# Kernel optimization log

Measured on AMD Instinct MI355X. Metric: run time of the kernel, lower is better.

The kernel has to match this reference:

```python
import jax, jax.numpy as jnp
import numpy as np
import math

B, T, E, H = 4, 4096, 1024, 16
D = E // H  # head dim
EPS_DENOM = 1e-6
LN_EPS = 1e-5


def setup_inputs() -> dict:
    key = jax.random.key(0)
    ks = jax.random.split(key, 8)
    s = 0.02
    return {
        "x": jax.random.normal(ks[0], (B, T, E), jnp.float32),
        "ln1_w": jnp.ones((E,), jnp.float32),
        "ln1_b": jnp.zeros((E,), jnp.float32),
        "wq": jax.random.normal(ks[1], (E, E), jnp.float32) * s,
        "bq": jnp.zeros((E,), jnp.float32),
        "wk": jax.random.normal(ks[2], (E, E), jnp.float32) * s,
        "bk": jnp.zeros((E,), jnp.float32),
        "wv": jax.random.normal(ks[3], (E, E), jnp.float32) * s,
        "bv": jnp.zeros((E,), jnp.float32),
        "wo": jax.random.normal(ks[4], (E, E), jnp.float32) * s,
        "bo": jnp.zeros((E,), jnp.float32),
        "ln2_w": jnp.ones((E,), jnp.float32),
        "ln2_b": jnp.zeros((E,), jnp.float32),
        "w_fc": jax.random.normal(ks[5], (E, 4 * E), jnp.float32) * s,
        "b_fc": jnp.zeros((4 * E,), jnp.float32),
        "w_proj": jax.random.normal(ks[6], (4 * E, E), jnp.float32) * s,
        "b_proj": jnp.zeros((E,), jnp.float32),
    }


def _layernorm(x, w, b):
    mu = jnp.mean(x, axis=-1, keepdims=True)
    var = jnp.mean(jnp.square(x - mu), axis=-1, keepdims=True)
    return (x - mu) * jax.lax.rsqrt(var + LN_EPS) * w + b


def _cosformer_attn(x, wq, bq, wk, bk, wv, bv, wo, bo):
    # ReLU feature map on q, k projections
    q = jax.nn.relu(x @ wq + bq)  # [B,T,E]
    k = jax.nn.relu(x @ wk + bk)
    v = x @ wv + bv
    # split heads -> [B,H,T,D]
    q = q.reshape(B, T, H, D).transpose(0, 2, 1, 3)
    k = k.reshape(B, T, H, D).transpose(0, 2, 1, 3)
    v = v.reshape(B, T, H, D).transpose(0, 2, 1, 3)
    # cosine reweighting: idx_i = pi/2 * (i+1)/M, M = T (self-attention)
    idx = (math.pi / 2.0) * jnp.arange(1, T + 1, dtype=x.dtype) / T  # [T]
    s = jnp.sin(idx)[None, None, :, None]
    c = jnp.cos(idx)[None, None, :, None]
    q_ = jnp.concatenate([q * s, q * c], axis=-1)  # [B,H,T,2D]
    k_ = jnp.concatenate([k * s, k * c], axis=-1)  # [B,H,T,2D]
    # non-causal linear attention: O = Q' (K'^T V) / (Q' K'^T 1)
    kv = jnp.einsum("bhtd,bhte->bhde", k_, v)       # [B,H,2D,D]
    z = 1.0 / jnp.maximum(jnp.einsum("bhtd,bhd->bht", q_, k_.sum(axis=2)), EPS_DENOM)
    out = jnp.einsum("bhtd,bhde,bht->bhte", q_, kv, z)  # [B,H,T,D]
    out = out.transpose(0, 2, 1, 3).reshape(B, T, E)
    return out @ wo + bo


def reference(x, ln1_w, ln1_b, wq, bq, wk, bk, wv, bv, wo, bo,
              ln2_w, ln2_b, w_fc, b_fc, w_proj, b_proj):
    h = _layernorm(x, ln1_w, ln1_b)
    x = x + _cosformer_attn(h, wq, bq, wk, bk, wv, bv, wo, bo)
    h = _layernorm(x, ln2_w, ln2_b)
    h = jax.nn.gelu(h @ w_fc + b_fc, approximate=False) @ w_proj + b_proj
    return x + h
```

## Files before the change

kernel.cpp:

```cpp
#include <hip/hip_runtime.h>

#define PI_F 3.14159265358979f
#define MT 16384
#define EE 1024
#define FF 4096
#define NCH 8
#define CHT (4096 / NCH)

typedef unsigned short u16;
typedef __attribute__((ext_vector_type(8))) short short8;
typedef __attribute__((ext_vector_type(4))) float f32x4;

__device__ __forceinline__ float bf2f(u16 u) {
  unsigned int v = ((unsigned int)u) << 16;
  float f;
  __builtin_memcpy(&f, &v, 4);
  return f;
}
__device__ __forceinline__ u16 f2bf(float f) {
  unsigned int x;
  __builtin_memcpy(&x, &f, 4);
  unsigned int r = x + 0x7fffu + ((x >> 16) & 1u);
  return (u16)(r >> 16);
}
__device__ __forceinline__ float ldin(const void* p, long i, int f32) {
  return f32 ? ((const float*)p)[i] : bf2f(((const u16*)p)[i]);
}
__device__ __forceinline__ void async16(const u16* g, u16* l) {
  __builtin_amdgcn_global_load_lds(
      (const __attribute__((address_space(1))) unsigned int*)g,
      (__attribute__((address_space(3))) unsigned int*)l, 16, 0, 0);
}

__global__ __launch_bounds__(256) void detect_dtype(const u16* __restrict__ x,
                                                    int* __restrict__ flag) {
  const int tid = threadIdx.x;
  int cnt = 0;
  for (int i = tid; i < 2048; i += 256) {
    const int e = (x[i] >> 7) & 0xFF;
    if (e == 0 || e >= 0x90) cnt++;
  }
#pragma unroll
  for (int o = 32; o > 0; o >>= 1) cnt += __shfl_xor(cnt, o);
  __shared__ int s[4];
  if ((tid & 63) == 0) s[tid >> 6] = cnt;
  __syncthreads();
  if (tid == 0) flag[0] = (s[0] + s[1] + s[2] + s[3] > 200) ? 1 : 0;
}

__global__ __launch_bounds__(256) void transpose_in(
    const void* __restrict__ src, const int* __restrict__ flag,
    u16* __restrict__ dst, int R, int C) {
  __shared__ float tile[64][65];
  const int f = *flag;
  const int tx = threadIdx.x & 63, ty = threadIdx.x >> 6;
  const long c0 = (long)blockIdx.x * 64, r0 = (long)blockIdx.y * 64;
#pragma unroll
  for (int i = 0; i < 16; i++) {
    const int r = ty + i * 4;
    tile[r][tx] = ldin(src, (r0 + r) * (long)C + c0 + tx, f);
  }
  __syncthreads();
#pragma unroll
  for (int i = 0; i < 16; i++) {
    const int cc = ty + i * 4;
    dst[(c0 + cc) * (long)R + r0 + tx] = f2bf(tile[tx][cc]);
  }
}

__global__ __launch_bounds__(256) void concat3(
    const void* __restrict__ a, const void* __restrict__ b,
    const void* __restrict__ c, const int* __restrict__ flag,
    float* __restrict__ out) {
  const int i = blockIdx.x * 256 + threadIdx.x;
  const int fl = *flag;
  if (i < 1024) out[i] = ldin(a, i, fl);
  else if (i < 2048) out[i] = ldin(b, i - 1024, fl);
  else if (i < 3072) out[i] = ldin(c, i - 2048, fl);
}

__global__ __launch_bounds__(256) void ln_kernel(
    const void* __restrict__ xin, int xmode, const int* __restrict__ flag,
    const void* __restrict__ w, const void* __restrict__ b,
    u16* __restrict__ out) {
  const long row = blockIdx.x;
  const int tid = threadIdx.x;
  const int fl = *flag;
  const int xf = (xmode == 2) ? fl : xmode;
  float v[4];
  if (xf) {
    const float4 q = ((const float4*)((const float*)xin + row * EE))[tid];
    v[0] = q.x; v[1] = q.y; v[2] = q.z; v[3] = q.w;
  } else {
    const ushort4 u = ((const ushort4*)((const u16*)xin + row * EE))[tid];
    v[0] = bf2f(u.x); v[1] = bf2f(u.y); v[2] = bf2f(u.z); v[3] = bf2f(u.w);
  }
  float sum = v[0] + v[1] + v[2] + v[3];
  float sq = v[0] * v[0] + v[1] * v[1] + v[2] * v[2] + v[3] * v[3];
#pragma unroll
  for (int o = 32; o > 0; o >>= 1) {
    sum += __shfl_xor(sum, o);
    sq += __shfl_xor(sq, o);
  }
  __shared__ float s1[4], s2[4];
  const int wave = tid >> 6, lane = tid & 63;
  if (lane == 0) { s1[wave] = sum; s2[wave] = sq; }
  __syncthreads();
  sum = s1[0] + s1[1] + s1[2] + s1[3];
  sq = s2[0] + s2[1] + s2[2] + s2[3];
  const float mu = sum * (1.f / EE);
  const float var = sq * (1.f / EE) - mu * mu;
  const float rs = rsqrtf(var + 1e-5f);
  ushort4 o4;
  float r0 = (v[0] - mu) * rs * ldin(w, tid * 4 + 0, fl) + ldin(b, tid * 4 + 0, fl);
  float r1 = (v[1] - mu) * rs * ldin(w, tid * 4 + 1, fl) + ldin(b, tid * 4 + 1, fl);
  float r2 = (v[2] - mu) * rs * ldin(w, tid * 4 + 2, fl) + ldin(b, tid * 4 + 2, fl);
  float r3 = (v[3] - mu) * rs * ldin(w, tid * 4 + 3, fl) + ldin(b, tid * 4 + 3, fl);
  o4.x = f2bf(r0); o4.y = f2bf(r1); o4.z = f2bf(r2); o4.w = f2bf(r3);
  ((ushort4*)(out + row * EE))[tid] = o4;
}

__global__ __launch_bounds__(256) void gemm_bf16(
    const u16* __restrict__ A, const u16* __restrict__ Bt,
    const void* __restrict__ bias, int biasF32,
    const void* __restrict__ res, int resMode,
    void* __restrict__ Cout, void* __restrict__ Cv, int outMode, long coff,
    const int* __restrict__ flag, int M, int N, int K, int act) {
  __shared__ u16 As[2][128 * 32];
  __shared__ u16 Bs[2][128 * 32];
  const int tid = threadIdx.x;
  const int lane = tid & 63;
  const int wave = tid >> 6;
  const int quad = lane >> 4;
  const int l16 = lane & 15;
  const int wm = (wave >> 1) * 64;
  const int wn = (wave & 1) * 64;
  const long bm = (long)blockIdx.x * 128;
  const long bn = (long)blockIdx.y * 128;

  f32x4 acc[4][4];
#pragma unroll
  for (int i = 0; i < 4; i++)
#pragma unroll
    for (int j = 0; j < 4; j++)
#pragma unroll
      for (int r = 0; r < 4; r++) acc[i][j][r] = 0.f;

  const int srow = tid >> 2;
  const int scol = (tid & 3) * 8;
  const u16* Ap = A + (bm + srow) * (long)K + scol;
  const u16* Bp = Bt + (bn + srow) * (long)K + scol;
  const long K64 = (long)64 * K;
  u16* As0 = &As[0][0];
  u16* Bs0 = &Bs[0][0];

  auto stage = [&](int b) {
    u16* Ad = As0 + b * 4096 + wave * 512;
    u16* Bd = Bs0 + b * 4096 + wave * 512;
    async16(Ap, Ad);
    async16(Ap + K64, Ad + 2048);
    async16(Bp, Bd);
    async16(Bp + K64, Bd + 2048);
    Ap += 32;
    Bp += 32;
  };
  auto compute = [&](int b) {
    const u16* Ab = As0 + b * 4096;
    const u16* Bb = Bs0 + b * 4096;
    short8 af[4], bfr[4];
#pragma unroll
    for (int i = 0; i < 4; i++)
      af[i] = *(const short8*)&Ab[(wm + i * 16 + l16) * 32 + quad * 8];
#pragma unroll
    for (int i = 0; i < 4; i++)
      bfr[i] = *(const short8*)&Bb[(wn + i * 16 + l16) * 32 + quad * 8];
#pragma unroll
    for (int mi = 0; mi < 4; mi++)
#pragma unroll
      for (int ni = 0; ni < 4; ni++)
        acc[mi][ni] = __builtin_amdgcn_mfma_f32_16x16x32_bf16(
            af[mi], bfr[ni], acc[mi][ni], 0, 0, 0);
  };

  stage(0);
  __syncthreads();
  const int nk = K >> 5;
  int buf = 0;
  for (int t = 1; t < nk; t++) {
    stage(buf ^ 1);
    compute(buf);
    __syncthreads();
    buf ^= 1;
  }
  compute(buf);

  const int fl = *flag;
#pragma unroll
  for (int ni = 0; ni < 4; ni++) {
    const long gc = bn + wn + ni * 16 + l16;
    const float bvv = biasF32 ? ((const float*)bias)[gc] : ldin(bias, gc, fl);
#pragma unroll
    for (int mi = 0; mi < 4; mi++) {
      const long gr0 = bm + wm + mi * 16 + quad * 4;
#pragma unroll
      for (int r = 0; r < 4; r++) {
        float val = acc[mi][ni][r] + bvv;
        if (act == 1 || (act == 3 && gc < 2048)) val = fmaxf(val, 0.f);
        else if (act == 2) val = 0.5f * val * (1.f + erff(val * 0.70710678118654752f));
        const long row = gr0 + r;
        if (outMode == 3) {
          const long plane = gc >> 10;
          u16* dst = (plane == 2) ? (u16*)Cv
                                  : ((u16*)Cout + plane * ((long)M << 10));
          dst[(row << 10) + (gc & 1023)] = f2bf(val);
        } else {
          const long idx = row * (long)N + gc;
          float v2 = val;
          if (resMode == 1) v2 += ((const float*)res)[idx];
          else if (resMode == 2) v2 += ldin(res, idx, fl);
          if (outMode == 1 || (outMode == 2 && fl)) ((float*)Cout)[coff + idx] = v2;
          else ((u16*)Cout)[coff + idx] = f2bf(v2);
        }
      }
    }
  }
}

__global__ __launch_bounds__(256) void kv_partial(
    const u16* __restrict__ k, const u16* __restrict__ v,
    float* __restrict__ kvpart, float* __restrict__ kspart) {
  const int bh = blockIdx.x;
  const int ch = blockIdx.y;
  const int b = bh >> 4, h = bh & 15;
  const int tid = threadIdx.x;
  __shared__ float kl[8][64], vl[8][64];
  const int dkq = tid >> 4;
  const int dvq = tid & 15;
  float accS[4][4] = {}, accC[4][4] = {};
  float ksS[4] = {}, ksC[4] = {};
  const int tt = tid >> 5;
  const int cc = (tid & 31) * 2;
  const long base = ((long)b * 4096 + ch * CHT) * EE + h * 64;
  for (int tb = 0; tb < CHT; tb += 8) {
    const long roff = base + (long)(tb + tt) * EE + cc;
    const unsigned int ku = *(const unsigned int*)(k + roff);
    const unsigned int vu = *(const unsigned int*)(v + roff);
    __syncthreads();
    kl[tt][cc] = bf2f((u16)ku);
    kl[tt][cc + 1] = bf2f((u16)(ku >> 16));
    vl[tt][cc] = bf2f((u16)vu);
    vl[tt][cc + 1] = bf2f((u16)(vu >> 16));
    __syncthreads();
#pragma unroll
    for (int j = 0; j < 8; j++) {
      const int t = ch * CHT + tb + j;
      float s, c;
      __sincosf((float)(t + 1) * (PI_F * 0.5f / 4096.f), &s, &c);
      float kk[4], vv[4];
#pragma unroll
      for (int i = 0; i < 4; i++) {
        kk[i] = kl[j][dkq * 4 + i];
        vv[i] = vl[j][dvq * 4 + i];
      }
#pragma unroll
      for (int i = 0; i < 4; i++) {
        const float ks_ = kk[i] * s, kc_ = kk[i] * c;
        ksS[i] += ks_;
        ksC[i] += kc_;
#pragma unroll
        for (int jj = 0; jj < 4; jj++) {
          accS[i][jj] += ks_ * vv[jj];
          accC[i][jj] += kc_ * vv[jj];
        }
      }
    }
  }
  float* outS = kvpart + (((long)ch * 64 + bh) * 2 + 0) * 4096;
  float* outC = outS + 4096;
#pragma unroll
  for (int i = 0; i < 4; i++)
#pragma unroll
    for (int jj = 0; jj < 4; jj++) {
      outS[(dkq * 4 + i) * 64 + dvq * 4 + jj] = accS[i][jj];
      outC[(dkq * 4 + i) * 64 + dvq * 4 + jj] = accC[i][jj];
    }
  if (dvq == 0) {
    float* oS = kspart + ((long)ch * 64 + bh) * 2 * 64;
#pragma unroll
    for (int i = 0; i < 4; i++) {
      oS[dkq * 4 + i] = ksS[i];
      oS[64 + dkq * 4 + i] = ksC[i];
    }
  }
}

__global__ __launch_bounds__(256) void kv_reduce(
    const float* __restrict__ kvpart, const float* __restrict__ kspart,
    float* __restrict__ kvcomb, float* __restrict__ kscomb) {
  const long KVTOT = 64L * 2 * 4096;
  const long KSTOT = 64L * 2 * 64;
  const long idx = (long)blockIdx.x * 256 + threadIdx.x;
  if (idx < KVTOT) {
    float s = 0.f;
#pragma unroll
    for (int chn = 0; chn < NCH; chn++) s += kvpart[chn * KVTOT + idx];
    kvcomb[idx] = s;
  } else {
    const long i2 = idx - KVTOT;
    if (i2 < KSTOT) {
      float s = 0.f;
#pragma unroll
      for (int chn = 0; chn < NCH; chn++) s += kspart[chn * KSTOT + i2];
      kscomb[i2] = s;
    }
  }
}

__global__ __launch_bounds__(256) void attn_apply(
    const u16* __restrict__ q, const float* __restrict__ kvcomb,
    const float* __restrict__ kscomb, u16* __restrict__ attn) {
  const int bh = blockIdx.x;
  const int b = bh >> 4, h = bh & 15;
  const int t0 = blockIdx.y * 64;
  const int tid = threadIdx.x;
  __shared__ float kvl[2][64][64];
  __shared__ float ksl[2][64];
  __shared__ float ql[64][66];

  const float4* kvsrc = (const float4*)(kvcomb + (long)bh * 8192);
  float4* kvdst = (float4*)&kvl[0][0][0];
#pragma unroll
  for (int i = 0; i < 8; i++) kvdst[tid + 256 * i] = kvsrc[tid + 256 * i];
  if (tid < 32) ((float4*)&ksl[0][0])[tid] = ((const float4*)(kscomb + (long)bh * 128))[tid];
  {
    const int r = tid >> 2;
    const int c = (tid & 3) * 16;
    const u16* qp = q + ((long)b * 4096 + t0 + r) * EE + h * 64 + c;
    const uint4 u0 = *(const uint4*)qp;
    const uint4 u1 = *(const uint4*)(qp + 8);
    unsigned int uu[8] = {u0.x, u0.y, u0.z, u0.w, u1.x, u1.y, u1.z, u1.w};
#pragma unroll
    for (int i = 0; i < 8; i++) {
      ql[r][c + 2 * i] = bf2f((u16)uu[i]);
      ql[r][c + 2 * i + 1] = bf2f((u16)(uu[i] >> 16));
    }
  }
  __syncthreads();

  const int tg = tid >> 4;
  const int dvq = tid & 15;
  const int dv0 = dvq * 4;

  float o1[4][4] = {}, o2[4][4] = {}, zs[4] = {}, zc[4] = {};
  for (int dk = 0; dk < 64; dk++) {
    const float ks0 = ksl[0][dk], ks1 = ksl[1][dk];
    float kv0[4], kv1[4];
#pragma unroll
    for (int j = 0; j < 4; j++) {
      kv0[j] = kvl[0][dk][dv0 + j];
      kv1[j] = kvl[1][dk][dv0 + j];
    }
#pragma unroll
    for (int it = 0; it < 4; it++) {
      const float qv = ql[tg + it * 16][dk];
      zs[it] += qv * ks0;
      zc[it] += qv * ks1;
#pragma unroll
      for (int j = 0; j < 4; j++) {
        o1[it][j] += qv * kv0[j];
        o2[it][j] += qv * kv1[j];
      }
    }
  }
#pragma unroll
  for (int it = 0; it < 4; it++) {
    const int t = t0 + tg + it * 16;
    float s, c;
    __sincosf((float)(t + 1) * (PI_F * 0.5f / 4096.f), &s, &c);
    const float z = s * zs[it] + c * zc[it];
    const float zinv = 1.f / fmaxf(z, 1e-6f);
    ushort4 o4;
    o4.x = f2bf((s * o1[it][0] + c * o2[it][0]) * zinv);
    o4.y = f2bf((s * o1[it][1] + c * o2[it][1]) * zinv);
    o4.z = f2bf((s * o1[it][2] + c * o2[it][2]) * zinv);
    o4.w = f2bf((s * o1[it][3] + c * o2[it][3]) * zinv);
    *(ushort4*)(attn + ((long)b * 4096 + t) * EE + h * 64 + dv0) = o4;
  }
}

extern "C" void kernel_launch(void* const* d_in, const int* in_sizes, int n_in,
                              void* d_out, int out_size, void* d_ws, size_t ws_size,
                              hipStream_t stream) {
  const void* x = d_in[0];
  const void* ln1w = d_in[1];
  const void* ln1b = d_in[2];
  const void* wq = d_in[3];
  const void* bq = d_in[4];
  const void* wk = d_in[5];
  const void* bk = d_in[6];
  const void* wv = d_in[7];
  const void* bv = d_in[8];
  const void* wo = d_in[9];
  const void* bo = d_in[10];
  const void* ln2w = d_in[11];
  const void* ln2b = d_in[12];
  const void* wfc = d_in[13];
  const void* bfc = d_in[14];
  const void* wproj = d_in[15];
  const void* bproj = d_in[16];

  char* ws = (char*)d_ws;
  size_t off = 0;
  auto alloc = [&](size_t bytes) -> char* {
    char* p = ws + off;
    off += (bytes + 255) & ~((size_t)255);
    return p;
  };
  int* flag = (int*)alloc(256);
  u16* wqkvT = (u16*)alloc((size_t)3 * EE * EE * 2);
  u16* woT = (u16*)alloc((size_t)EE * EE * 2);
  u16* wfcT = (u16*)alloc((size_t)EE * FF * 2);
  u16* wprojT = (u16*)alloc((size_t)FF * EE * 2);
  float* qkvBias = (float*)alloc(3072 * 4);
  u16* h = (u16*)alloc((size_t)MT * EE * 2);
  float* x2 = (float*)alloc((size_t)MT * EE * 4);
  u16* qk2 = (u16*)alloc((size_t)2 * MT * EE * 2);
  float* kvpart = (float*)alloc((size_t)NCH * 64 * 2 * 64 * 64 * 4);
  float* kspart = (float*)alloc((size_t)NCH * 64 * 2 * 64 * 4);
  float* kvcomb = (float*)alloc((size_t)64 * 2 * 64 * 64 * 4);
  float* kscomb = (float*)alloc((size_t)64 * 2 * 64 * 4);
  const long PL = (long)MT * EE;
  u16* qb = qk2;
  u16* kb = qk2 + PL;
  u16* vb = (u16*)x2;
  u16* attnb = kb;
  u16* g = qk2;
  (void)ws_size; (void)in_sizes; (void)n_in; (void)out_size;

  detect_dtype<<<1, 256, 0, stream>>>((const u16*)x, flag);

  transpose_in<<<dim3(16, 16), 256, 0, stream>>>(wq, flag, wqkvT, EE, EE);
  transpose_in<<<dim3(16, 16), 256, 0, stream>>>(wk, flag, wqkvT + (size_t)EE * EE, EE, EE);
  transpose_in<<<dim3(16, 16), 256, 0, stream>>>(wv, flag, wqkvT + (size_t)2 * EE * EE, EE, EE);
  transpose_in<<<dim3(16, 16), 256, 0, stream>>>(wo, flag, woT, EE, EE);
  transpose_in<<<dim3(64, 16), 256, 0, stream>>>(wfc, flag, wfcT, EE, FF);
  transpose_in<<<dim3(16, 64), 256, 0, stream>>>(wproj, flag, wprojT, FF, EE);
  concat3<<<12, 256, 0, stream>>>(bq, bk, bv, flag, qkvBias);

  ln_kernel<<<MT, 256, 0, stream>>>(x, 2, flag, ln1w, ln1b, h);

  gemm_bf16<<<dim3(128, 24), 256, 0, stream>>>(h, wqkvT, qkvBias, 1, nullptr, 0,
                                               qk2, vb, 3, 0, flag, MT, 3072, EE, 3);

  kv_partial<<<dim3(64, NCH), 256, 0, stream>>>(kb, vb, kvpart, kspart);
  kv_reduce<<<2080, 256, 0, stream>>>(kvpart, kspart, kvcomb, kscomb);
  attn_apply<<<dim3(64, 64), 256, 0, stream>>>(qb, kvcomb, kscomb, attnb);

  gemm_bf16<<<dim3(128, 8), 256, 0, stream>>>(attnb, woT, bo, 0, x, 2, x2, nullptr,
                                              1, 0, flag, MT, EE, EE, 0);
  ln_kernel<<<MT, 256, 0, stream>>>(x2, 1, flag, ln2w, ln2b, h);

  for (int c = 0; c < 2; c++) {
    const long ro = (long)c * 8192 * EE;
    gemm_bf16<<<dim3(64, 32), 256, 0, stream>>>(h + ro, wfcT, bfc, 0, nullptr, 0,
                                                g, nullptr, 0, 0, flag, 8192, FF, EE, 2);
    gemm_bf16<<<dim3(64, 8), 256, 0, stream>>>(g, wprojT, bproj, 0, x2 + ro, 1,
                                               d_out, nullptr, 2, ro, flag, 8192, EE, FF, 0);
  }
}
```

Before: 1.290 ms.

## Deepen GEMM pipeline to 4 LDS stages with swizzle, XCD remap, vectorized epilogue

```diff
diff --git a/kernel.cpp b/kernel.cpp
--- a/kernel.cpp
+++ b/kernel.cpp
@@ -120,14 +120,14 @@
   ((ushort4*)(out + row * EE))[tid] = o4;
 }
 
-__global__ __launch_bounds__(256) void gemm_bf16(
+__global__ __launch_bounds__(256, 2) void gemm_bf16(
     const u16* __restrict__ A, const u16* __restrict__ Bt,
     const void* __restrict__ bias, int biasF32,
     const void* __restrict__ res, int resMode,
     void* __restrict__ Cout, void* __restrict__ Cv, int outMode, long coff,
     const int* __restrict__ flag, int M, int N, int K, int act) {
-  __shared__ u16 As[2][128 * 32];
-  __shared__ u16 Bs[2][128 * 32];
+  __shared__ u16 As[4][4096];
+  __shared__ u16 Bs[4][4096];
   const int tid = threadIdx.x;
   const int lane = tid & 63;
   const int wave = tid >> 6;
@@ -135,8 +135,13 @@
   const int l16 = lane & 15;
   const int wm = (wave >> 1) * 64;
   const int wn = (wave & 1) * 64;
-  const long bm = (long)blockIdx.x * 128;
-  const long bn = (long)blockIdx.y * 128;
+  const int nwg = gridDim.x * gridDim.y;
+  const int bid0 = blockIdx.x + gridDim.x * blockIdx.y;
+  const int bid = (bid0 & 7) * (nwg >> 3) + (bid0 >> 3);
+  const int bx = bid % gridDim.x;
+  const int by = bid / gridDim.x;
+  const long bm = (long)bx * 128;
+  const long bn = (long)by * 128;
 
   f32x4 acc[4][4];
 #pragma unroll
@@ -146,82 +151,132 @@
 #pragma unroll
       for (int r = 0; r < 4; r++) acc[i][j][r] = 0.f;
 
-  const int srow = tid >> 2;
-  const int scol = (tid & 3) * 8;
-  const u16* Ap = A + (bm + srow) * (long)K + scol;
-  const u16* Bp = Bt + (bn + srow) * (long)K + scol;
-  const long K64 = (long)64 * K;
-  u16* As0 = &As[0][0];
-  u16* Bs0 = &Bs[0][0];
-
-  auto stage = [&](int b) {
-    u16* Ad = As0 + b * 4096 + wave * 512;
-    u16* Bd = Bs0 + b * 4096 + wave * 512;
-    async16(Ap, Ad);
-    async16(Ap + K64, Ad + 2048);
-    async16(Bp, Bd);
-    async16(Bp + K64, Bd + 2048);
-    Ap += 32;
-    Bp += 32;
+  const int trow = tid >> 2;
+  const int tswz = (tid & 3) ^ (trow & 3);
+  const u16* Ap = A + (bm + trow) * (long)K + tswz * 8;
+  const u16* Bp = Bt + (bn + trow) * (long)K + tswz * 8;
+  const long rowK64 = 64 * (long)K;
+
+  auto stage = [&](int buf, long kt) {
+    u16* Ad = &As[buf][wave * 512];
+    u16* Bd = &Bs[buf][wave * 512];
+    async16(Ap + kt, Ad);
+    async16(Ap + rowK64 + kt, Ad + 2048);
+    async16(Bp + kt, Bd);
+    async16(Bp + rowK64 + kt, Bd + 2048);
   };
-  auto compute = [&](int b) {
-    const u16* Ab = As0 + b * 4096;
-    const u16* Bb = Bs0 + b * 4096;
+  const int rswz = (quad ^ (l16 & 3)) * 8;
+  auto compute = [&](int buf) {
     short8 af[4], bfr[4];
 #pragma unroll
     for (int i = 0; i < 4; i++)
-      af[i] = *(const short8*)&Ab[(wm + i * 16 + l16) * 32 + quad * 8];
+      af[i] = *(const short8*)&As[buf][(wm + i * 16 + l16) * 32 + rswz];
 #pragma unroll
     for (int i = 0; i < 4; i++)
-      bfr[i] = *(const short8*)&Bb[(wn + i * 16 + l16) * 32 + quad * 8];
+      bfr[i] = *(const short8*)&Bs[buf][(wn + i * 16 + l16) * 32 + rswz];
+    __builtin_amdgcn_s_setprio(1);
 #pragma unroll
     for (int mi = 0; mi < 4; mi++)
 #pragma unroll
       for (int ni = 0; ni < 4; ni++)
         acc[mi][ni] = __builtin_amdgcn_mfma_f32_16x16x32_bf16(
             af[mi], bfr[ni], acc[mi][ni], 0, 0, 0);
+    __builtin_amdgcn_s_setprio(0);
   };
 
-  stage(0);
+  const int nt = K >> 5;
+  stage(0, 0);
+  stage(1, 32);
+  stage(2, 64);
+  asm volatile("s_waitcnt vmcnt(8)" ::: "memory");
+  __builtin_amdgcn_s_barrier();
+  for (int t = 0; t < nt; ++t) {
+    const long ts = (t + 3 < nt) ? (long)(t + 3) : (long)(nt - 1);
+    stage((t + 3) & 3, ts * 32);
+    compute(t & 3);
+    asm volatile("s_waitcnt vmcnt(8)" ::: "memory");
+    __builtin_amdgcn_s_barrier();
+  }
   __syncthreads();
-  const int nk = K >> 5;
-  int buf = 0;
-  for (int t = 1; t < nk; t++) {
-    stage(buf ^ 1);
-    compute(buf);
-    __syncthreads();
-    buf ^= 1;
-  }
-  compute(buf);
 
   const int fl = *flag;
+  const long Nl = N;
+  float bv4[4];
+  long gcA[4];
 #pragma unroll
   for (int ni = 0; ni < 4; ni++) {
-    const long gc = bn + wn + ni * 16 + l16;
-    const float bvv = biasF32 ? ((const float*)bias)[gc] : ldin(bias, gc, fl);
-#pragma unroll
-    for (int mi = 0; mi < 4; mi++) {
-      const long gr0 = bm + wm + mi * 16 + quad * 4;
+    gcA[ni] = bn + wn + ni * 16 + l16;
+    bv4[ni] = biasF32 ? ((const float*)bias)[gcA[ni]] : ldin(bias, gcA[ni], fl);
+  }
+#pragma unroll
+  for (int mi = 0; mi < 4; mi++)
+#pragma unroll
+    for (int ni = 0; ni < 4; ni++)
 #pragma unroll
       for (int r = 0; r < 4; r++) {
-        float val = acc[mi][ni][r] + bvv;
-        if (act == 1 || (act == 3 && gc < 2048)) val = fmaxf(val, 0.f);
-        else if (act == 2) val = 0.5f * val * (1.f + erff(val * 0.70710678118654752f));
-        const long row = gr0 + r;
-        if (outMode == 3) {
-          const long plane = gc >> 10;
-          u16* dst = (plane == 2) ? (u16*)Cv
-                                  : ((u16*)Cout + plane * ((long)M << 10));
-          dst[(row << 10) + (gc & 1023)] = f2bf(val);
-        } else {
-          const long idx = row * (long)N + gc;
-          float v2 = val;
-          if (resMode == 1) v2 += ((const float*)res)[idx];
-          else if (resMode == 2) v2 += ldin(res, idx, fl);
-          if (outMode == 1 || (outMode == 2 && fl)) ((float*)Cout)[coff + idx] = v2;
-          else ((u16*)Cout)[coff + idx] = f2bf(v2);
-        }
-      }
+        float v = acc[mi][ni][r] + bv4[ni];
+        if (act == 1 || (act == 3 && gcA[ni] < 2048)) v = fmaxf(v, 0.f);
+        else if (act == 2) v = 0.5f * v * (1.f + erff(v * 0.70710678118654752f));
+        acc[mi][ni][r] = v;
+      }
+  float* sf = (float*)&As[0][0] + wave * 1088;
+  const int er = lane >> 2;
+  const int ec = (lane & 3) * 16;
+#pragma unroll
+  for (int mi = 0; mi < 4; mi++) {
+#pragma unroll
+    for (int ni = 0; ni < 4; ni++)
+#pragma unroll
+      for (int r = 0; r < 4; r++)
+        sf[(quad * 4 + r) * 68 + ni * 16 + l16] = acc[mi][ni][r];
+    f32x4 w0 = *(const f32x4*)&sf[er * 68 + ec + 0];
+    f32x4 w1 = *(const f32x4*)&sf[er * 68 + ec + 4];
+    f32x4 w2 = *(const f32x4*)&sf[er * 68 + ec + 8];
+    f32x4 w3 = *(const f32x4*)&sf[er * 68 + ec + 12];
+    const long gr = bm + wm + mi * 16 + er;
+    const long gc0 = bn + wn + ec;
+    const long ib = gr * Nl + gc0;
+    if (resMode == 1 || (resMode == 2 && fl)) {
+      const f32x4* rp = (const f32x4*)((const float*)res + ib);
+      f32x4 r0 = rp[0], r1 = rp[1], r2 = rp[2], r3 = rp[3];
+#pragma unroll
+      for (int j = 0; j < 4; j++) {
+        w0[j] += r0[j]; w1[j] += r1[j]; w2[j] += r2[j]; w3[j] += r3[j];
+      }
+    } else if (resMode == 2) {
+      const short8* rp = (const short8*)((const u16*)res + ib);
+      short8 ra = rp[0], rb = rp[1];
+#pragma unroll
+      for (int j = 0; j < 4; j++) {
+        w0[j] += bf2f((u16)ra[j]);
+        w1[j] += bf2f((u16)ra[j + 4]);
+        w2[j] += bf2f((u16)rb[j]);
+        w3[j] += bf2f((u16)rb[j + 4]);
+      }
+    }
+    if (outMode == 1 || (outMode == 2 && fl)) {
+      f32x4* op = (f32x4*)((float*)Cout + coff + ib);
+      op[0] = w0; op[1] = w1; op[2] = w2; op[3] = w3;
+    } else {
+      u16 tmp[16];
+#pragma unroll
+      for (int j = 0; j < 4; j++) {
+        tmp[j] = f2bf(w0[j]);
+        tmp[j + 4] = f2bf(w1[j]);
+        tmp[j + 8] = f2bf(w2[j]);
+        tmp[j + 12] = f2bf(w3[j]);
+      }
+      u16* op;
+      if (outMode == 3) {
+        const int plane = (int)(bn >> 10);
+        u16* dst = (plane == 2) ? (u16*)Cv
+                                : ((u16*)Cout + plane * ((long)M << 10));
+        op = dst + (gr << 10) + (gc0 & 1023);
+      } else {
+        op = (u16*)Cout + coff + ib;
+      }
+      *(short8*)op = *(short8*)&tmp[0];
+      *(short8*)(op + 8) = *(short8*)&tmp[8];
     }
   }
 }
```

Result: no change. 1.292 ms (+0.2%).
